# Optimization experiments

Measured on AMD Instinct MI355X. Metric: run time of the kernel, lower is better.

Reference implementation:

```python
import jax, jax.numpy as jnp
import numpy as np

E = 1024        # embedding_dim
H = 16          # num_heads
DR = 1          # downsample_rate
INT = E // DR   # internal_dim
HD = INT // H   # head dim
B, NQ, NK = 4, 2048, 2048


def setup_inputs() -> dict:
    key = jax.random.key(0)
    ks = jax.random.split(key, 11)
    s_in = 1.0 / np.sqrt(E)
    s_int = 1.0 / np.sqrt(INT)
    return {
        "q": jax.random.normal(ks[0], (B, NQ, E), jnp.float32),
        "k": jax.random.normal(ks[1], (B, NK, E), jnp.float32),
        "v": jax.random.normal(ks[2], (B, NK, E), jnp.float32),
        "wq": jax.random.normal(ks[3], (E, INT), jnp.float32) * s_in,
        "bq": jnp.zeros((INT,), jnp.float32),
        "wk": jax.random.normal(ks[4], (E, INT), jnp.float32) * s_in,
        "bk": jnp.zeros((INT,), jnp.float32),
        "wv": jax.random.normal(ks[5], (E, INT), jnp.float32) * s_in,
        "bv": jnp.zeros((INT,), jnp.float32),
        "wo": jax.random.normal(ks[6], (INT, E), jnp.float32) * s_int,
        "bo": jnp.zeros((E,), jnp.float32),
    }


def _heads(x):
    # (B, N, INT) -> (B, H, N, HD)
    b, n, c = x.shape
    return x.reshape(b, n, H, c // H).transpose(0, 2, 1, 3)


def reference(q, k, v, wq, bq, wk, bk, wv, bv, wo, bo):
    qh = _heads(q @ wq + bq)          # (B,H,NQ,HD)
    kh = _heads(k @ wk + bk)          # (B,H,NK,HD)
    vh = _heads(v @ wv + bv)          # (B,H,NK,HD)
    scale = 1.0 / np.sqrt(HD)
    attn = jnp.einsum('bhqd,bhkd->bhqk', qh, kh) * scale  # (B,H,NQ,NK)
    attn = jax.nn.softmax(attn, axis=-1)
    out = jnp.einsum('bhqk,bhkd->bhqd', attn, vh)          # (B,H,NQ,HD)
    out = out.transpose(0, 2, 1, 3).reshape(q.shape[0], qh.shape[2], INT)
    return out @ wo + bo
```

## Files before the change

### kernel.cpp

```cpp
#include <hip/hip_runtime.h>
#include <hip/hip_bf16.h>
#include <cstdint>
#include <cstddef>

typedef __bf16 bf16_t;
typedef __bf16 bf16x8 __attribute__((ext_vector_type(8)));
typedef float f32x4 __attribute__((ext_vector_type(4)));
typedef float f32x16 __attribute__((ext_vector_type(16)));
typedef uint32_t u32;

#define EDIM 1024
#define HH 16
#define HD 64
#define NSEQ 2048
#define QSCALE 0.18033688011f

__device__ __forceinline__ void async_copy16(const bf16_t* gsrc, bf16_t* lds_dst) {
    __builtin_amdgcn_global_load_lds(
        (const __attribute__((address_space(1))) uint32_t*)gsrc,
        (__attribute__((address_space(3))) uint32_t*)lds_dst,
        16, 0, 0);
}

__global__ void transpose_all(const float* __restrict__ w0, const float* __restrict__ w1,
                              const float* __restrict__ w2, const float* __restrict__ w3,
                              bf16_t* __restrict__ o0, bf16_t* __restrict__ o1,
                              bf16_t* __restrict__ o2, bf16_t* __restrict__ o3) {
    __shared__ bf16_t t[64][65];
    const float* in;
    bf16_t* out;
    switch (blockIdx.z) {
        case 0: in = w0; out = o0; break;
        case 1: in = w1; out = o1; break;
        case 2: in = w2; out = o2; break;
        default: in = w3; out = o3; break;
    }
    const int tid = threadIdx.x;
    const int kt = blockIdx.x, nt = blockIdx.y;
    #pragma unroll
    for (int i = 0; i < 16; i++) {
        int idx = i * 256 + tid;
        int r = idx >> 6, c = idx & 63;
        t[r][c] = (bf16_t)in[(size_t)(kt * 64 + r) * 1024 + nt * 64 + c];
    }
    __syncthreads();
    #pragma unroll
    for (int i = 0; i < 16; i++) {
        int idx = i * 256 + tid;
        int r = idx >> 6, c = idx & 63;
        out[(size_t)(nt * 64 + r) * 1024 + kt * 64 + c] = t[c][r];
    }
}

__global__ __launch_bounds__(256, 4)
void gemm_qkv(const float* __restrict__ Aq, const float* __restrict__ Ak,
              const float* __restrict__ Av,
              const bf16_t* __restrict__ Wq, const bf16_t* __restrict__ Wk,
              const bf16_t* __restrict__ Wv,
              const float* __restrict__ bq, const float* __restrict__ bk,
              const float* __restrict__ bv,
              bf16_t* __restrict__ Qh, bf16_t* __restrict__ Kh,
              bf16_t* __restrict__ Vt) {
    constexpr int BM = 128, BN = 128, BK = 32, K = 1024, NT = K / BK;
    __shared__ bf16_t Asm[BM * BK];
    __shared__ bf16_t Bsm[BN * BK];
    const int tid = threadIdx.x;
    const int wave = tid >> 6, lane = tid & 63;
    const int quad = lane >> 4, l15 = lane & 15;
    const int bx = blockIdx.x, by = blockIdx.y;
    const int mt = (by >> 3) * 8 + bx;
    const int n0 = (by & 7) * BN;
    const int wt = mt >> 6;
    const int m0 = (mt - wt * 64) * BM;
    const int wm = (wave & 1) * 64, wn = (wave >> 1) * 64;

    const float*  A    = wt == 0 ? Aq : (wt == 1 ? Ak : Av);
    const bf16_t* Bt   = wt == 0 ? Wq : (wt == 1 ? Wk : Wv);
    const float*  bias = wt == 0 ? bq : (wt == 1 ? bk : bv);
    bf16_t*       Cout = wt == 0 ? Qh : (wt == 1 ? Kh : Vt);
    const float oscale = wt == 0 ? QSCALE : 1.0f;

    f32x4 acc[4][4] = {};

    for (int t = 0; t < NT; t++) {
        const int k0 = t * BK;
        __syncthreads();
        #pragma unroll
        for (int i = 0; i < 2; i++) {
            int s = i * 256 + tid;
            int row = s >> 2, c = s & 3;
            int kc = c ^ ((row >> 1) & 3);
            const float* sp = A + (size_t)(m0 + row) * K + k0 + kc * 8;
            float4 x = *(const float4*)sp;
            float4 y = *(const float4*)(sp + 4);
            bf16x8 vv = {(bf16_t)x.x, (bf16_t)x.y, (bf16_t)x.z, (bf16_t)x.w,
                         (bf16_t)y.x, (bf16_t)y.y, (bf16_t)y.z, (bf16_t)y.w};
            *(bf16x8*)&Asm[s * 8] = vv;
        }
        #pragma unroll
        for (int i = 0; i < 2; i++) {
            int s = i * 256 + tid;
            int row = s >> 2, c = s & 3;
            int kc = c ^ ((row >> 1) & 3);
            async_copy16(Bt + (size_t)(n0 + row) * K + k0 + kc * 8, Bsm + s * 8);
        }
        __syncthreads();

        bf16x8 af[4], bfr[4];
        #pragma unroll
        for (int mi = 0; mi < 4; mi++) {
            int row = wm + mi * 16 + l15;
            af[mi] = *(const bf16x8*)&Asm[row * BK + ((quad ^ ((row >> 1) & 3)) * 8)];
        }
        #pragma unroll
        for (int ni = 0; ni < 4; ni++) {
            int row = wn + ni * 16 + l15;
            bfr[ni] = *(const bf16x8*)&Bsm[row * BK + ((quad ^ ((row >> 1) & 3)) * 8)];
        }
        #pragma unroll
        for (int mi = 0; mi < 4; mi++)
            #pragma unroll
            for (int ni = 0; ni < 4; ni++)
                acc[mi][ni] = __builtin_amdgcn_mfma_f32_16x16x32_bf16(
                    af[mi], bfr[ni], acc[mi][ni], 0, 0, 0);
    }

    #pragma unroll
    for (int mi = 0; mi < 4; mi++) {
        #pragma unroll
        for (int ni = 0; ni < 4; ni++) {
            #pragma unroll
            for (int r = 0; r < 4; r++) {
                int m = m0 + wm + mi * 16 + quad * 4 + r;
                int nch = n0 + wn + ni * 16 + l15;
                float v = (acc[mi][ni][r] + bias[nch]) * oscale;
                int b = m >> 11, n = m & 2047;
                int h = nch >> 6, d = nch & 63;
                if (wt < 2)
                    Cout[(((size_t)(b * HH + h)) * NSEQ + n) * HD + d] = (bf16_t)v;
                else
                    Cout[(((size_t)(b * HH + h)) * HD + d) * NSEQ + n] = (bf16_t)v;
            }
        }
    }
}

__global__ __launch_bounds__(256, 4)
void gemm_out(const bf16_t* __restrict__ A, const bf16_t* __restrict__ Bt,
              const float* __restrict__ bias, float* __restrict__ C) {
    constexpr int BM = 128, BN = 128, BK = 32, K = 1024, N = 1024, NT = K / BK;
    __shared__ bf16_t Asm[BM * BK];
    __shared__ bf16_t Bsm[BN * BK];
    const int tid = threadIdx.x;
    const int wave = tid >> 6, lane = tid & 63;
    const int quad = lane >> 4, l15 = lane & 15;
    const int bx = blockIdx.x, by = blockIdx.y;
    const int n0 = (by & 7) * BN;
    const int m0 = ((by >> 3) * 8 + bx) * BM;
    const int wm = (wave & 1) * 64, wn = (wave >> 1) * 64;

    f32x4 acc[4][4] = {};

    for (int t = 0; t < NT; t++) {
        const int k0 = t * BK;
        __syncthreads();
        #pragma unroll
        for (int i = 0; i < 2; i++) {
            int s = i * 256 + tid;
            int row = s >> 2, c = s & 3;
            int kc = c ^ ((row >> 1) & 3);
            async_copy16(A + (size_t)(m0 + row) * K + k0 + kc * 8, Asm + s * 8);
        }
        #pragma unroll
        for (int i = 0; i < 2; i++) {
            int s = i * 256 + tid;
            int row = s >> 2, c = s & 3;
            int kc = c ^ ((row >> 1) & 3);
            async_copy16(Bt + (size_t)(n0 + row) * K + k0 + kc * 8, Bsm + s * 8);
        }
        __syncthreads();

        bf16x8 af[4], bfr[4];
        #pragma unroll
        for (int mi = 0; mi < 4; mi++) {
            int row = wm + mi * 16 + l15;
            af[mi] = *(const bf16x8*)&Asm[row * BK + ((quad ^ ((row >> 1) & 3)) * 8)];
        }
        #pragma unroll
        for (int ni = 0; ni < 4; ni++) {
            int row = wn + ni * 16 + l15;
            bfr[ni] = *(const bf16x8*)&Bsm[row * BK + ((quad ^ ((row >> 1) & 3)) * 8)];
        }
        #pragma unroll
        for (int mi = 0; mi < 4; mi++)
            #pragma unroll
            for (int ni = 0; ni < 4; ni++)
                acc[mi][ni] = __builtin_amdgcn_mfma_f32_16x16x32_bf16(
                    af[mi], bfr[ni], acc[mi][ni], 0, 0, 0);
    }

    #pragma unroll
    for (int mi = 0; mi < 4; mi++) {
        #pragma unroll
        for (int ni = 0; ni < 4; ni++) {
            #pragma unroll
            for (int r = 0; r < 4; r++) {
                int m = m0 + wm + mi * 16 + quad * 4 + r;
                int nch = n0 + wn + ni * 16 + l15;
                C[(size_t)m * N + nch] = acc[mi][ni][r] + bias[nch];
            }
        }
    }
}

union PW { u32 w[4]; bf16x8 v; };

__device__ __forceinline__ u32 pack_bf16(float lo, float hi) {
    union { bf16_t h[2]; u32 u; } x;
    x.h[0] = (bf16_t)lo;
    x.h[1] = (bf16_t)hi;
    return x.u;
}

__device__ __forceinline__ void half_swap(u32& a, u32& b) {
    auto r = __builtin_amdgcn_permlane32_swap(a, b, false, false);
    a = r[0];
    b = r[1];
}

__device__ __forceinline__ void softmax_pack(const f32x16 sa, float* lp,
                                             PW& f0, PW& f1) {
    float p[16];
    #pragma unroll
    for (int r = 0; r < 16; r++) {
        p[r] = __builtin_amdgcn_exp2f(sa[r]);
        lp[r & 3] += p[r];
    }
    u32 x0 = pack_bf16(p[0],  p[1]),  x1 = pack_bf16(p[2],  p[3]);
    u32 x2 = pack_bf16(p[4],  p[5]),  x3 = pack_bf16(p[6],  p[7]);
    u32 x4 = pack_bf16(p[8],  p[9]),  x5 = pack_bf16(p[10], p[11]);
    u32 x6 = pack_bf16(p[12], p[13]), x7 = pack_bf16(p[14], p[15]);
    half_swap(x0, x2); half_swap(x1, x3);
    half_swap(x4, x6); half_swap(x5, x7);
    f0.w[0] = x0; f0.w[1] = x1; f0.w[2] = x2; f0.w[3] = x3;
    f1.w[0] = x4; f1.w[1] = x5; f1.w[2] = x6; f1.w[3] = x7;
}

__global__ __launch_bounds__(256, 2)
void attn_kernel(const bf16_t* __restrict__ Qh, const bf16_t* __restrict__ Kh,
                 const bf16_t* __restrict__ Vt, bf16_t* __restrict__ out) {
    __shared__ bf16_t Ks[2][64 * 64];
    __shared__ bf16_t Vs[2][64 * 64];
    const int tid = threadIdx.x, wave = tid >> 6, lane = tid & 63;
    const int l31 = lane & 31, hi = lane >> 5;
    const int B = blockIdx.x;
    const int qt = (B >> 3) & 15;
    const int bh = (B >> 7) * 8 + (B & 7);
    const int b = bh >> 4, h = bh & 15;

    const bf16_t* kbase = Kh + (size_t)bh * NSEQ * HD;
    const bf16_t* vbase = Vt + (size_t)bh * HD * NSEQ;

    bf16x8 qf[4];
    {
        const bf16_t* qrow =
            Qh + ((size_t)bh * NSEQ + qt * 128 + wave * 32 + l31) * HD + hi * 8;
        #pragma unroll
        for (int s = 0; s < 4; s++) qf[s] = *(const bf16x8*)(qrow + s * 16);
    }

    const bf16_t *ks0, *ks1, *vs0, *vs1;
    {
        int r0 = tid >> 3, c0 = tid & 7;
        int s1 = tid + 256;
        int r1 = s1 >> 3, c1 = s1 & 7;
        ks0 = kbase + r0 * HD + (c0 ^ (r0 & 7)) * 8;
        ks1 = kbase + r1 * HD + (c1 ^ (r1 & 7)) * 8;
        vs0 = vbase + (size_t)r0 * NSEQ + (c0 ^ (r0 & 7)) * 8;
        vs1 = vbase + (size_t)r1 * NSEQ + (c1 ^ (r1 & 7)) * 8;
    }

    async_copy16(ks0, &Ks[0][tid * 8]);
    async_copy16(ks1, &Ks[0][(tid + 256) * 8]);
    async_copy16(vs0, &Vs[0][tid * 8]);
    async_copy16(vs1, &Vs[0][(tid + 256) * 8]);

    f32x16 oacc[2] = {};
    float lp[4] = {};

    for (int t = 0; t < 32; t++) {
        const int cur = t & 1;
        __syncthreads();

        if (t < 31) {
            ks0 += 64 * HD; ks1 += 64 * HD;
            vs0 += 64;      vs1 += 64;
            async_copy16(ks0, &Ks[cur ^ 1][tid * 8]);
            async_copy16(ks1, &Ks[cur ^ 1][(tid + 256) * 8]);
            async_copy16(vs0, &Vs[cur ^ 1][tid * 8]);
            async_copy16(vs1, &Vs[cur ^ 1][(tid + 256) * 8]);
        }

        const f32x16 zero = {};
        f32x16 sacc0, sacc1;
        {
            int g = hi;
            int row0 = l31, row1 = 32 + l31;
            bf16x8 ak0 = *(const bf16x8*)&Ks[cur][row0 * 64 + ((g ^ (row0 & 7)) * 8)];
            bf16x8 ak1 = *(const bf16x8*)&Ks[cur][row1 * 64 + ((g ^ (row1 & 7)) * 8)];
            __builtin_amdgcn_s_setprio(1);
            sacc0 = __builtin_amdgcn_mfma_f32_32x32x16_bf16(ak0, qf[0], zero, 0, 0, 0);
            sacc1 = __builtin_amdgcn_mfma_f32_32x32x16_bf16(ak1, qf[0], zero, 0, 0, 0);
            __builtin_amdgcn_s_setprio(0);
        }
        #pragma unroll
        for (int s = 1; s < 4; s++) {
            int g = s * 2 + hi;
            int row0 = l31;
            int row1 = 32 + l31;
            bf16x8 ak0 = *(const bf16x8*)&Ks[cur][row0 * 64 + ((g ^ (row0 & 7)) * 8)];
            bf16x8 ak1 = *(const bf16x8*)&Ks[cur][row1 * 64 + ((g ^ (row1 & 7)) * 8)];
            __builtin_amdgcn_s_setprio(1);
            sacc0 = __builtin_amdgcn_mfma_f32_32x32x16_bf16(ak0, qf[s], sacc0, 0, 0, 0);
            sacc1 = __builtin_amdgcn_mfma_f32_32x32x16_bf16(ak1, qf[s], sacc1, 0, 0, 0);
            __builtin_amdgcn_s_setprio(0);
        }

        PW pa[4];
        softmax_pack(sacc0, lp, pa[0], pa[1]);
        softmax_pack(sacc1, lp, pa[2], pa[3]);

        #pragma unroll
        for (int dt = 0; dt < 2; dt++) {
            #pragma unroll
            for (int ks = 0; ks < 4; ks++) {
                int row = dt * 32 + l31;
                int g = ks * 2 + hi;
                bf16x8 bv = *(const bf16x8*)&Vs[cur][row * 64 + ((g ^ (row & 7)) * 8)];
                __builtin_amdgcn_s_setprio(1);
                oacc[dt] = __builtin_amdgcn_mfma_f32_32x32x16_bf16(
                    pa[ks].v, bv, oacc[dt], 0, 0, 0);
                __builtin_amdgcn_s_setprio(0);
            }
        }
    }

    float lsum = (lp[0] + lp[1]) + (lp[2] + lp[3]);
    lsum += __shfl_xor(lsum, 32, 64);
    float linv = 1.f / lsum;
    float rinv[16];
    #pragma unroll
    for (int r = 0; r < 16; r++) {
        int q = (r & 3) + 8 * (r >> 2) + 4 * hi;
        rinv[r] = __shfl(linv, q, 64);
    }

    const int n0 = qt * 128 + wave * 32;
    #pragma unroll
    for (int dt = 0; dt < 2; dt++) {
        int c = h * 64 + dt * 32 + l31;
        #pragma unroll
        for (int r = 0; r < 16; r++) {
            int q = (r & 3) + 8 * (r >> 2) + 4 * hi;
            out[((size_t)b * NSEQ + n0 + q) * EDIM + c] = (bf16_t)(oacc[dt][r] * rinv[r]);
        }
    }
}

extern "C" void kernel_launch(void* const* d_in, const int* in_sizes, int n_in,
                              void* d_out, int out_size, void* d_ws, size_t ws_size,
                              hipStream_t stream) {
    const float* q  = (const float*)d_in[0];
    const float* k  = (const float*)d_in[1];
    const float* v  = (const float*)d_in[2];
    const float* wq = (const float*)d_in[3];
    const float* bq = (const float*)d_in[4];
    const float* wk = (const float*)d_in[5];
    const float* bk = (const float*)d_in[6];
    const float* wv = (const float*)d_in[7];
    const float* bv = (const float*)d_in[8];
    const float* wo = (const float*)d_in[9];
    const float* bo = (const float*)d_in[10];
    float* out = (float*)d_out;

    char* ws = (char*)d_ws;
    bf16_t* wqt = (bf16_t*)(ws + ((size_t)0  << 20));
    bf16_t* wkt = (bf16_t*)(ws + ((size_t)2  << 20));
    bf16_t* wvt = (bf16_t*)(ws + ((size_t)4  << 20));
    bf16_t* wot = (bf16_t*)(ws + ((size_t)6  << 20));

    bf16_t* Qh  = (bf16_t*)(ws + ((size_t)8  << 20));
    bf16_t* Kh  = (bf16_t*)(ws + ((size_t)24 << 20));
    bf16_t* Vt  = (bf16_t*)(ws + ((size_t)40 << 20));
    bf16_t* ao  = (bf16_t*)(ws + ((size_t)56 << 20));

    dim3 tb(256);

    transpose_all<<<dim3(16, 16, 4), tb, 0, stream>>>(wq, wk, wv, wo, wqt, wkt, wvt, wot);

    gemm_qkv<<<dim3(8, 192), tb, 0, stream>>>(q, k, v, wqt, wkt, wvt,
                                              bq, bk, bv, Qh, Kh, Vt);

    attn_kernel<<<1024, tb, 0, stream>>>(Qh, Kh, Vt, ao);

    gemm_out<<<dim3(8, 64), tb, 0, stream>>>(ao, wot, bo, out);
}
```

Measured before the change: 374.7 us.

## Add 4-buffer, 2-ahead async prefetch pipelines to GEMM and attention kernels

```diff
diff --git a/kernel.cpp b/kernel.cpp
--- a/kernel.cpp
+++ b/kernel.cpp
@@ -20,6 +20,12 @@
         (const __attribute__((address_space(1))) uint32_t*)gsrc,
         (__attribute__((address_space(3))) uint32_t*)lds_dst,
         16, 0, 0);
+}
+
+__device__ __forceinline__ bf16x8 cvt8(float4 x, float4 y) {
+    bf16x8 v = {(bf16_t)x.x, (bf16_t)x.y, (bf16_t)x.z, (bf16_t)x.w,
+                (bf16_t)y.x, (bf16_t)y.y, (bf16_t)y.z, (bf16_t)y.w};
+    return v;
 }
 
 __global__ void transpose_all(const float* __restrict__ w0, const float* __restrict__ w1,
@@ -52,7 +58,7 @@
     }
 }
 
-__global__ __launch_bounds__(256, 4)
+__global__ __launch_bounds__(256, 2)
 void gemm_qkv(const float* __restrict__ Aq, const float* __restrict__ Ak,
               const float* __restrict__ Av,
               const bf16_t* __restrict__ Wq, const bf16_t* __restrict__ Wk,
@@ -62,8 +68,8 @@
               bf16_t* __restrict__ Qh, bf16_t* __restrict__ Kh,
               bf16_t* __restrict__ Vt) {
     constexpr int BM = 128, BN = 128, BK = 32, K = 1024, NT = K / BK;
-    __shared__ bf16_t Asm[BM * BK];
-    __shared__ bf16_t Bsm[BN * BK];
+    __shared__ bf16_t Asm[4][BM * BK];
+    __shared__ bf16_t Bsm[4][BN * BK];
     const int tid = threadIdx.x;
     const int wave = tid >> 6, lane = tid & 63;
     const int quad = lane >> 4, l15 = lane & 15;
@@ -80,49 +86,70 @@
     bf16_t*       Cout = wt == 0 ? Qh : (wt == 1 ? Kh : Vt);
     const float oscale = wt == 0 ? QSCALE : 1.0f;
 
+    const int s0 = tid, s1 = 256 + tid;
+    const int row0 = s0 >> 2, kc0 = (s0 & 3) ^ ((row0 >> 1) & 3);
+    const int row1 = s1 >> 2, kc1 = (s1 & 3) ^ ((row1 >> 1) & 3);
+    const float*  a0 = A  + (size_t)(m0 + row0) * K + kc0 * 8;
+    const float*  a1 = A  + (size_t)(m0 + row1) * K + kc1 * 8;
+    const bf16_t* b0 = Bt + (size_t)(n0 + row0) * K + kc0 * 8;
+    const bf16_t* b1 = Bt + (size_t)(n0 + row1) * K + kc1 * 8;
+
     f32x4 acc[4][4] = {};
-
-    for (int t = 0; t < NT; t++) {
-        const int k0 = t * BK;
-        __syncthreads();
-        #pragma unroll
-        for (int i = 0; i < 2; i++) {
-            int s = i * 256 + tid;
-            int row = s >> 2, c = s & 3;
-            int kc = c ^ ((row >> 1) & 3);
-            const float* sp = A + (size_t)(m0 + row) * K + k0 + kc * 8;
-            float4 x = *(const float4*)sp;
-            float4 y = *(const float4*)(sp + 4);
-            bf16x8 vv = {(bf16_t)x.x, (bf16_t)x.y, (bf16_t)x.z, (bf16_t)x.w,
-                         (bf16_t)y.x, (bf16_t)y.y, (bf16_t)y.z, (bf16_t)y.w};
-            *(bf16x8*)&Asm[s * 8] = vv;
-        }
-        #pragma unroll
-        for (int i = 0; i < 2; i++) {
-            int s = i * 256 + tid;
-            int row = s >> 2, c = s & 3;
-            int kc = c ^ ((row >> 1) & 3);
-            async_copy16(Bt + (size_t)(n0 + row) * K + k0 + kc * 8, Bsm + s * 8);
-        }
-        __syncthreads();
+    float4 ar[4];
+
+    auto loadA = [&](int tt) {
+        ar[0] = *(const float4*)(a0 + tt * BK);
+        ar[1] = *(const float4*)(a0 + tt * BK + 4);
+        ar[2] = *(const float4*)(a1 + tt * BK);
+        ar[3] = *(const float4*)(a1 + tt * BK + 4);
+    };
+    auto writeA = [&](int buf) {
+        *(bf16x8*)&Asm[buf][s0 * 8] = cvt8(ar[0], ar[1]);
+        *(bf16x8*)&Asm[buf][s1 * 8] = cvt8(ar[2], ar[3]);
+    };
+    auto stageB = [&](int tt, int buf) {
+        async_copy16(b0 + tt * BK, &Bsm[buf][s0 * 8]);
+        async_copy16(b1 + tt * BK, &Bsm[buf][s1 * 8]);
+    };
+
+    loadA(0);
+    stageB(0, 0);
+    stageB(1, 1);
+    writeA(0);
+    loadA(1);
+
+    for (int t = 0; t < NT; ++t) {
+        const int buf = t & 3;
+        if (t + 1 < NT) {
+            if (t + 2 < NT) stageB(t + 2, (t + 2) & 3);
+            writeA((t + 1) & 3);
+            if (t + 2 < NT) loadA(t + 2);
+            asm volatile("s_waitcnt lgkmcnt(0)" ::: "memory");
+        } else {
+            asm volatile("s_waitcnt vmcnt(0) lgkmcnt(0)" ::: "memory");
+        }
+        __builtin_amdgcn_s_barrier();
+        __builtin_amdgcn_sched_barrier(0);
 
         bf16x8 af[4], bfr[4];
         #pragma unroll
         for (int mi = 0; mi < 4; mi++) {
             int row = wm + mi * 16 + l15;
-            af[mi] = *(const bf16x8*)&Asm[row * BK + ((quad ^ ((row >> 1) & 3)) * 8)];
+            af[mi] = *(const bf16x8*)&Asm[buf][row * BK + ((quad ^ ((row >> 1) & 3)) * 8)];
         }
         #pragma unroll
         for (int ni = 0; ni < 4; ni++) {
             int row = wn + ni * 16 + l15;
-            bfr[ni] = *(const bf16x8*)&Bsm[row * BK + ((quad ^ ((row >> 1) & 3)) * 8)];
-        }
+            bfr[ni] = *(const bf16x8*)&Bsm[buf][row * BK + ((quad ^ ((row >> 1) & 3)) * 8)];
+        }
+        __builtin_amdgcn_s_setprio(1);
         #pragma unroll
         for (int mi = 0; mi < 4; mi++)
             #pragma unroll
             for (int ni = 0; ni < 4; ni++)
                 acc[mi][ni] = __builtin_amdgcn_mfma_f32_16x16x32_bf16(
                     af[mi], bfr[ni], acc[mi][ni], 0, 0, 0);
+        __builtin_amdgcn_s_setprio(0);
     }
 
     #pragma unroll
@@ -145,12 +172,12 @@
     }
 }
 
-__global__ __launch_bounds__(256, 4)
+__global__ __launch_bounds__(256, 2)
 void gemm_out(const bf16_t* __restrict__ A, const bf16_t* __restrict__ Bt,
               const float* __restrict__ bias, float* __restrict__ C) {
     constexpr int BM = 128, BN = 128, BK = 32, K = 1024, N = 1024, NT = K / BK;
-    __shared__ bf16_t Asm[BM * BK];
-    __shared__ bf16_t Bsm[BN * BK];
+    __shared__ bf16_t Asm[4][BM * BK];
+    __shared__ bf16_t Bsm[4][BN * BK];
     const int tid = threadIdx.x;
     const int wave = tid >> 6, lane = tid & 63;
     const int quad = lane >> 4, l15 = lane & 15;
@@ -159,44 +186,58 @@
     const int m0 = ((by >> 3) * 8 + bx) * BM;
     const int wm = (wave & 1) * 64, wn = (wave >> 1) * 64;
 
+    const int s0 = tid, s1 = 256 + tid;
+    const int row0 = s0 >> 2, kc0 = (s0 & 3) ^ ((row0 >> 1) & 3);
+    const int row1 = s1 >> 2, kc1 = (s1 & 3) ^ ((row1 >> 1) & 3);
+    const bf16_t* a0 = A  + (size_t)(m0 + row0) * K + kc0 * 8;
+    const bf16_t* a1 = A  + (size_t)(m0 + row1) * K + kc1 * 8;
+    const bf16_t* b0 = Bt + (size_t)(n0 + row0) * K + kc0 * 8;
+    const bf16_t* b1 = Bt + (size_t)(n0 + row1) * K + kc1 * 8;
+
     f32x4 acc[4][4] = {};
 
-    for (int t = 0; t < NT; t++) {
-        const int k0 = t * BK;
-        __syncthreads();
-        #pragma unroll
-        for (int i = 0; i < 2; i++) {
-            int s = i * 256 + tid;
-            int row = s >> 2, c = s & 3;
-            int kc = c ^ ((row >> 1) & 3);
-            async_copy16(A + (size_t)(m0 + row) * K + k0 + kc * 8, Asm + s * 8);
-        }
-        #pragma unroll
-        for (int i = 0; i < 2; i++) {
-            int s = i * 256 + tid;
-            int row = s >> 2, c = s & 3;
-            int kc = c ^ ((row >> 1) & 3);
-            async_copy16(Bt + (size_t)(n0 + row) * K + k0 + kc * 8, Bsm + s * 8);
-        }
-        __syncthreads();
+    auto stage = [&](int tt, int buf) {
+        async_copy16(a0 + tt * BK, &Asm[buf][s0 * 8]);
+        async_copy16(a1 + tt * BK, &Asm[buf][s1 * 8]);
+        async_copy16(b0 + tt * BK, &Bsm[buf][s0 * 8]);
+        async_copy16(b1 + tt * BK, &Bsm[buf][s1 * 8]);
+    };
+
+    stage(0, 0);
+    stage(1, 1);
+
+    for (int t = 0; t < NT; ++t) {
+        const int buf = t & 3;
+        if (t + 2 < NT) {
+            stage(t + 2, (t + 2) & 3);
+            asm volatile("s_waitcnt vmcnt(8)" ::: "memory");
+        } else if (t + 1 < NT) {
+            asm volatile("s_waitcnt vmcnt(4)" ::: "memory");
+        } else {
+            asm volatile("s_waitcnt vmcnt(0)" ::: "memory");
+        }
+        __builtin_amdgcn_s_barrier();
+        __builtin_amdgcn_sched_barrier(0);
 
         bf16x8 af[4], bfr[4];
         #pragma unroll
         for (int mi = 0; mi < 4; mi++) {
             int row = wm + mi * 16 + l15;
-            af[mi] = *(const bf16x8*)&Asm[row * BK + ((quad ^ ((row >> 1) & 3)) * 8)];
+            af[mi] = *(const bf16x8*)&Asm[buf][row * BK + ((quad ^ ((row >> 1) & 3)) * 8)];
         }
         #pragma unroll
         for (int ni = 0; ni < 4; ni++) {
             int row = wn + ni * 16 + l15;
-            bfr[ni] = *(const bf16x8*)&Bsm[row * BK + ((quad ^ ((row >> 1) & 3)) * 8)];
-        }
+            bfr[ni] = *(const bf16x8*)&Bsm[buf][row * BK + ((quad ^ ((row >> 1) & 3)) * 8)];
+        }
+        __builtin_amdgcn_s_setprio(1);
         #pragma unroll
         for (int mi = 0; mi < 4; mi++)
             #pragma unroll
             for (int ni = 0; ni < 4; ni++)
                 acc[mi][ni] = __builtin_amdgcn_mfma_f32_16x16x32_bf16(
                     af[mi], bfr[ni], acc[mi][ni], 0, 0, 0);
+        __builtin_amdgcn_s_setprio(0);
     }
 
     #pragma unroll
@@ -249,8 +290,8 @@
 __global__ __launch_bounds__(256, 2)
 void attn_kernel(const bf16_t* __restrict__ Qh, const bf16_t* __restrict__ Kh,
                  const bf16_t* __restrict__ Vt, bf16_t* __restrict__ out) {
-    __shared__ bf16_t Ks[2][64 * 64];
-    __shared__ bf16_t Vs[2][64 * 64];
+    __shared__ bf16_t Ks[4][64 * 64];
+    __shared__ bf16_t Vs[4][64 * 64];
     const int tid = threadIdx.x, wave = tid >> 6, lane = tid & 63;
     const int l31 = lane & 31, hi = lane >> 5;
     const int B = blockIdx.x;
@@ -269,45 +310,46 @@
         for (int s = 0; s < 4; s++) qf[s] = *(const bf16x8*)(qrow + s * 16);
     }
 
-    const bf16_t *ks0, *ks1, *vs0, *vs1;
-    {
-        int r0 = tid >> 3, c0 = tid & 7;
-        int s1 = tid + 256;
-        int r1 = s1 >> 3, c1 = s1 & 7;
-        ks0 = kbase + r0 * HD + (c0 ^ (r0 & 7)) * 8;
-        ks1 = kbase + r1 * HD + (c1 ^ (r1 & 7)) * 8;
-        vs0 = vbase + (size_t)r0 * NSEQ + (c0 ^ (r0 & 7)) * 8;
-        vs1 = vbase + (size_t)r1 * NSEQ + (c1 ^ (r1 & 7)) * 8;
-    }
-
-    async_copy16(ks0, &Ks[0][tid * 8]);
-    async_copy16(ks1, &Ks[0][(tid + 256) * 8]);
-    async_copy16(vs0, &Vs[0][tid * 8]);
-    async_copy16(vs1, &Vs[0][(tid + 256) * 8]);
+    int r0 = tid >> 3, c0 = tid & 7;
+    int r1 = (tid + 256) >> 3, c1 = tid & 7;
+    const size_t ko0 = (size_t)r0 * HD + (c0 ^ (r0 & 7)) * 8;
+    const size_t ko1 = (size_t)r1 * HD + (c1 ^ (r1 & 7)) * 8;
+    const size_t vo0 = (size_t)r0 * NSEQ + (c0 ^ (r0 & 7)) * 8;
+    const size_t vo1 = (size_t)r1 * NSEQ + (c1 ^ (r1 & 7)) * 8;
+
+    auto stage = [&](int tt, int buf) {
+        async_copy16(kbase + (size_t)tt * 64 * HD + ko0, &Ks[buf][tid * 8]);
+        async_copy16(kbase + (size_t)tt * 64 * HD + ko1, &Ks[buf][(tid + 256) * 8]);
+        async_copy16(vbase + (size_t)tt * 64 + vo0, &Vs[buf][tid * 8]);
+        async_copy16(vbase + (size_t)tt * 64 + vo1, &Vs[buf][(tid + 256) * 8]);
+    };
+
+    stage(0, 0);
+    stage(1, 1);
 
     f32x16 oacc[2] = {};
     float lp[4] = {};
 
     for (int t = 0; t < 32; t++) {
-        const int cur = t & 1;
-        __syncthreads();
-
-        if (t < 31) {
-            ks0 += 64 * HD; ks1 += 64 * HD;
-            vs0 += 64;      vs1 += 64;
-            async_copy16(ks0, &Ks[cur ^ 1][tid * 8]);
-            async_copy16(ks1, &Ks[cur ^ 1][(tid + 256) * 8]);
-            async_copy16(vs0, &Vs[cur ^ 1][tid * 8]);
-            async_copy16(vs1, &Vs[cur ^ 1][(tid + 256) * 8]);
-        }
+        const int buf = t & 3;
+        if (t + 2 < 32) {
+            stage(t + 2, (t + 2) & 3);
+            asm volatile("s_waitcnt vmcnt(8)" ::: "memory");
+        } else if (t + 1 < 32) {
+            asm volatile("s_waitcnt vmcnt(4)" ::: "memory");
+        } else {
+            asm volatile("s_waitcnt vmcnt(0)" ::: "memory");
+        }
+        __builtin_amdgcn_s_barrier();
+        __builtin_amdgcn_sched_barrier(0);
 
         const f32x16 zero = {};
         f32x16 sacc0, sacc1;
         {
             int g = hi;
-            int row0 = l31, row1 = 32 + l31;
-            bf16x8 ak0 = *(const bf16x8*)&Ks[cur][row0 * 64 + ((g ^ (row0 & 7)) * 8)];
-            bf16x8 ak1 = *(const bf16x8*)&Ks[cur][row1 * 64 + ((g ^ (row1 & 7)) * 8)];
+            int row0_ = l31, row1_ = 32 + l31;
+            bf16x8 ak0 = *(const bf16x8*)&Ks[buf][row0_ * 64 + ((g ^ (row0_ & 7)) * 8)];
+            bf16x8 ak1 = *(const bf16x8*)&Ks[buf][row1_ * 64 + ((g ^ (row1_ & 7)) * 8)];
             __builtin_amdgcn_s_setprio(1);
             sacc0 = __builtin_amdgcn_mfma_f32_32x32x16_bf16(ak0, qf[0], zero, 0, 0, 0);
             sacc1 = __builtin_amdgcn_mfma_f32_32x32x16_bf16(ak1, qf[0], zero, 0, 0, 0);
@@ -316,10 +358,10 @@
         #pragma unroll
         for (int s = 1; s < 4; s++) {
             int g = s * 2 + hi;
-            int row0 = l31;
-            int row1 = 32 + l31;
-            bf16x8 ak0 = *(const bf16x8*)&Ks[cur][row0 * 64 + ((g ^ (row0 & 7)) * 8)];
-            bf16x8 ak1 = *(const bf16x8*)&Ks[cur][row1 * 64 + ((g ^ (row1 & 7)) * 8)];
+            int row0_ = l31;
+            int row1_ = 32 + l31;
+            bf16x8 ak0 = *(const bf16x8*)&Ks[buf][row0_ * 64 + ((g ^ (row0_ & 7)) * 8)];
+            bf16x8 ak1 = *(const bf16x8*)&Ks[buf][row1_ * 64 + ((g ^ (row1_ & 7)) * 8)];
             __builtin_amdgcn_s_setprio(1);
             sacc0 = __builtin_amdgcn_mfma_f32_32x32x16_bf16(ak0, qf[s], sacc0, 0, 0, 0);
             sacc1 = __builtin_amdgcn_mfma_f32_32x32x16_bf16(ak1, qf[s], sacc1, 0, 0, 0);
@@ -336,7 +378,7 @@
             for (int ks = 0; ks < 4; ks++) {
                 int row = dt * 32 + l31;
                 int g = ks * 2 + hi;
-                bf16x8 bv = *(const bf16x8*)&Vs[cur][row * 64 + ((g ^ (row & 7)) * 8)];
+                bf16x8 bv = *(const bf16x8*)&Vs[buf][row * 64 + ((g ^ (row & 7)) * 8)];
                 __builtin_amdgcn_s_setprio(1);
                 oacc[dt] = __builtin_amdgcn_mfma_f32_32x32x16_bf16(
                     pa[ks].v, bv, oacc[dt], 0, 0, 0);
```

Measured after the change: 376.2 us. Within noise of the previous version (+0.4%).
